# Kernel tuning notes

Measured on AMD Instinct MI355X. Metric: run time of the kernel, lower is better.

## Reference

```python
import jax, jax.numpy as jnp
import numpy as np

B, S1, S2, C = 8, 256, 256, 64
M1, M2 = 32, 32          # n_modes per spatial dim
SCALE = 1.0 / (C * C)    # 1/(in_channels*out_channels)


def setup_inputs() -> dict:
    key = jax.random.key(0)
    ks = jax.random.split(key, 5)
    X = jax.random.normal(ks[0], (B, S1, S2, C), dtype=jnp.float32)
    k0r = SCALE * jax.random.normal(ks[1], (M1, C, C), dtype=jnp.float32)
    k0i = SCALE * jax.random.normal(ks[2], (M1, C, C), dtype=jnp.float32)
    k1r = SCALE * jax.random.normal(ks[3], (M2, C, C), dtype=jnp.float32)
    k1i = SCALE * jax.random.normal(ks[4], (M2, C, C), dtype=jnp.float32)
    return {"X": X, "k0r": k0r, "k0i": k0i, "k1r": k1r, "k1i": k1i}


def reference(X, k0r, k0i, k1r, k1i):
    # Factorized spectral conv: per-spatial-dim rFFT -> truncated-mode
    # complex channel mix -> zero-pad -> irFFT, summed over dims.
    k0 = jax.lax.complex(k0r, k0i)  # (M1, out, in)
    k1 = jax.lax.complex(k1r, k1i)  # (M2, out, in)

    out = jnp.zeros_like(X)

    # --- spatial dim 0 (axis -3) ---
    Xf = jnp.fft.rfft(X, axis=-3, norm="forward")          # (B, S1//2+1, S2, C) complex
    Yt = jnp.einsum("rij,bryj->bryi", k0, Xf[:, :M1])       # truncated-mode channel mix
    Y = jnp.zeros_like(Xf).at[:, :M1].set(Yt)               # zero-pad back to full modes
    out = out + jnp.fft.irfft(Y, n=S1, axis=-3, norm="forward")

    # --- spatial dim 1 (axis -2) ---
    Xf = jnp.fft.rfft(X, axis=-2, norm="forward")           # (B, S1, S2//2+1, C)
    Yt = jnp.einsum("rij,bxrj->bxri", k1, Xf[:, :, :M2])
    Y = jnp.zeros_like(Xf).at[:, :, :M2].set(Yt)
    out = out + jnp.fft.irfft(Y, n=S2, axis=-2, norm="forward")

    return out
```

## Files before the change

### kernel.cpp

```cpp
#include <hip/hip_runtime.h>


namespace {

constexpr int S = 256, C = 64;

typedef _Float16 f16;
typedef _Float16 f16x2 __attribute__((ext_vector_type(2)));
typedef _Float16 f16x4 __attribute__((ext_vector_type(4)));
typedef _Float16 f16x8 __attribute__((ext_vector_type(8)));
typedef float f32x16 __attribute__((ext_vector_type(16)));

constexpr int OFF_FWDF = 0;
constexpr int OFF_INVF = 8192;
constexpr int OFF_A2   = 16384;

constexpr int P   = 4624;
constexpr int XFO = 8 * P;
constexpr int LDS_BYTES = 16 * P;

__device__ __host__ inline int cadr(int c) { return c * 16 + (c >> 3) * 16; }

__global__ void k_init_all(const float* __restrict__ k0r, const float* __restrict__ k0i,
                           const float* __restrict__ k1r, const float* __restrict__ ki1,
                           float* __restrict__ ws) {
  const int bid = blockIdx.x;
  if (bid < 128) {
    int t = bid * 256 + threadIdx.x;
    f16* fwdF = (f16*)(ws + OFF_FWDF);
    f16* invF = (f16*)(ws + OFF_INVF);
    if (t < 16384) {
      int e = t & 7, lane = (t >> 3) & 63, mtkk = t >> 9;
      int mt = mtkk & 1, kk = mtkk >> 1;
      int mc = mt * 32 + (lane & 31);
      int x = kk * 16 + 8 * (lane >> 5) + e;
      int r = mc >> 1;
      double ang = (double)((r * x) & 255) * (3.14159265358979323846 / 128.0);
      double v = (mc & 1) ? -sin(ang) : cos(ang);
      fwdF[t] = (f16)(float)v;
    } else {
      int t2 = t - 16384;
      int e = t2 & 7, lane = (t2 >> 3) & 63, mtg = (t2 >> 9) & 7, kk = t2 >> 12;
      int u = mtg * 32 + (lane & 31);
      int mcv = kk * 16 + 8 * (lane >> 5) + e;
      int r = mcv >> 1;
      double wgt = (r == 0) ? 1.0 : 2.0;
      double ang = (double)((r * u) & 255) * (3.14159265358979323846 / 128.0);
      double v = (mcv & 1) ? -wgt * sin(ang) : wgt * cos(ang);
      invF[t2] = (f16)(float)(v * (1.0 / 256.0));
    }
    return;
  }
  const int db = bid - 128;
  const float* kr = (db < 2048) ? k0r : k1r;
  const float* ki = (db < 2048) ? k0i : ki1;
  f16* A2 = (f16*)(ws + OFF_A2) + ((db < 2048) ? 0 : 524288);
  int t = (db & 2047) * 256 + threadIdx.x;
  int e = t & 7, l = (t >> 3) & 63, kk = (t >> 9) & 7, mt = (t >> 12) & 3, r = t >> 14;
  int m = mt * 32 + (l & 31);
  int kreal = kk * 16 + 8 * (l >> 5) + e;
  int i = m >> 1, imo = m & 1, j = kreal >> 1, imi = kreal & 1;
  int src = (r * 64 + i) * 64 + j;
  float v = (imi == 0) ? ((imo == 0) ? kr[src] : ki[src])
                       : ((imo == 0) ? -ki[src] : kr[src]);
  A2[t] = (f16)v;
}

template <int DIM>
__launch_bounds__(512, 2)
__global__ void k_dim(const float* __restrict__ X, const float* __restrict__ ws,
                      float* __restrict__ out) {
  __shared__ char sm[LDS_BYTES] __attribute__((aligned(16)));

  const int tid = threadIdx.x;
  const int l = tid & 63, w = tid >> 6;
  const int g2 = l >> 5, l31 = l & 31;
  const int n0 = w * 32;
  const int b = blockIdx.x >> 6;
  const int t4 = (blockIdx.x & 63) * 4;
  const size_t bbase = (size_t)b * (S * S * C);
  const f16* fwdF = (const f16*)(ws + OFF_FWDF);
  const f16* invF = (const f16*)(ws + OFF_INVF);
  const f16* A2 = (const f16*)(ws + OFF_A2) + (DIM == 0 ? 0 : 524288);

  auto gofs = [&](int u, int c) -> size_t {
    if (DIM == 0)
      return bbase + (size_t)u * (S * C) + (size_t)(t4 + (c >> 6)) * C + (c & 63);
    else
      return bbase + (size_t)(t4 + (c >> 6)) * (S * C) + (size_t)u * C + (c & 63);
  };

  const int ug = w >> 1;
  const int c1 = (w & 1) * 128 + l;
  const int c2 = c1 + 64;

  float r1[8], r2[8];
  auto stage_load = [&](int u0) {
#pragma unroll
    for (int j = 0; j < 8; ++j) r1[j] = X[gofs(u0 + ug * 8 + j, c1)];
#pragma unroll
    for (int j = 0; j < 8; ++j) r2[j] = X[gofs(u0 + ug * 8 + j, c2)];
  };
  auto stage_write = [&](int buf) {
    f16x8 v1, v2;
#pragma unroll
    for (int j = 0; j < 8; ++j) { v1[j] = (f16)r1[j]; v2[j] = (f16)r2[j]; }
    char* base = sm + buf * (4 * P) + ug * P;
    *(f16x8*)(base + cadr(c1)) = v1;
    *(f16x8*)(base + cadr(c2)) = v2;
  };

  f32x16 acc0, acc1;
#pragma unroll
  for (int q = 0; q < 16; ++q) { acc0[q] = 0.f; acc1[q] = 0.f; }

  stage_load(0);
  stage_write(0);
  __syncthreads();

  for (int ch = 0; ch < 8; ++ch) {
    if (ch < 7) stage_load((ch + 1) * 32);
    const char* bbuf = sm + (ch & 1) * (4 * P);
#pragma unroll
    for (int ks = 0; ks < 2; ++ks) {
      const int kk = ch * 2 + ks;
      f16x8 bf = *(const f16x8*)(bbuf + (ks * 2 + g2) * P + cadr(n0 + l31));
      f16x8 a0 = *(const f16x8*)(fwdF + ((size_t)(kk * 2 + 0) * 64 + l) * 8);
      f16x8 a1 = *(const f16x8*)(fwdF + ((size_t)(kk * 2 + 1) * 64 + l) * 8);
      acc0 = __builtin_amdgcn_mfma_f32_32x32x16_f16(a0, bf, acc0, 0, 0, 0);
      acc1 = __builtin_amdgcn_mfma_f32_32x32x16_f16(a1, bf, acc1, 0, 0, 0);
    }
    if (ch < 7) {
      stage_write((ch + 1) & 1);
      __syncthreads();
    }
  }
  __syncthreads();

  {
    const int col = n0 + l31;
    const int p = col >> 6, j = col & 63;
    const int kk = j >> 3, g2p = (j >> 2) & 1, js = j & 3;
#pragma unroll
    for (int pr = 0; pr < 16; ++pr) {
      const int q = (pr & 7) >> 1, hf = pr & 1;
      const int r = 2 * g2 + 4 * q + hf + (pr >> 3) * 16;
      const int reg = 4 * q + 2 * hf;
      const float v0 = (pr < 8) ? acc0[reg] : acc1[reg];
      const float v1 = (pr < 8) ? acc0[reg + 1] : acc1[reg + 1];
      f16x2 v2 = {(f16)v0, (f16)v1};
      const int W = (r * 16 + kk * 2 + g2p) * 4 + p;
      *(f16x2*)(sm + W * 16 + (W >> 3) * 16 + js * 4) = v2;
    }
  }
  __syncthreads();

  {
    const int colsel = l31 & 3;
#pragma unroll 1
    for (int rq = 0; rq < 4; ++rq) {
      const int r = w * 4 + rq;
      f16x8 bfr[8];
#pragma unroll
      for (int kk = 0; kk < 8; ++kk) {
        const int W = (r * 16 + kk * 2 + g2) * 4 + colsel;
        bfr[kk] = *(const f16x8*)(sm + W * 16 + (W >> 3) * 16);
      }
      char* yb = sm + XFO + w * P;
      const int ebyte = rq * 4;
#pragma unroll 1
      for (int mt = 0; mt < 4; ++mt) {
        f32x16 acc;
#pragma unroll
        for (int q = 0; q < 16; ++q) acc[q] = 0.f;
#pragma unroll
        for (int kk = 0; kk < 8; ++kk) {
          f16x8 af = *(const f16x8*)(A2 + ((size_t)((r * 4 + mt) * 8 + kk) * 64 + l) * 8);
          acc = __builtin_amdgcn_mfma_f32_32x32x16_f16(af, bfr[kk], acc, 0, 0, 0);
        }
        if (l31 < 4) {
#pragma unroll
          for (int t2 = 0; t2 < 8; ++t2) {
            int reg = t2 * 2;
            int rowin = (reg & 3) + 8 * (reg >> 2) + 4 * g2;
            int i = (mt * 32 + rowin) >> 1;
            f16x2 v2 = {(f16)acc[reg], (f16)acc[reg + 1]};
            *(f16x2*)(yb + cadr(l31 * 64 + i) + ebyte) = v2;
          }
        }
      }
    }
  }
  __syncthreads();

  const int colg = n0 + l31;
  const int pp = colg >> 6, jj = colg & 63;
  f16x8 bf4[4];
#pragma unroll
  for (int kk = 0; kk < 4; ++kk)
    bf4[kk] = *(const f16x8*)(sm + XFO + (kk * 2 + g2) * P + cadr(colg));

#pragma unroll 1
  for (int h = 0; h < 2; ++h) {
#pragma unroll 1
    for (int mt = 0; mt < 4; ++mt) {
      f32x16 a4;
#pragma unroll
      for (int q = 0; q < 16; ++q) a4[q] = 0.f;

#pragma unroll
      for (int kk = 0; kk < 4; ++kk) {
        f16x8 A = *(const f16x8*)(invF + ((size_t)(kk * 8 + h * 4 + mt) * 64 + l) * 8);
        a4 = __builtin_amdgcn_mfma_f32_32x32x16_f16(A, bf4[kk], a4, 0, 0, 0);
      }

      const int u0 = (h * 4 + mt) * 32;
#pragma unroll
      for (int reg = 0; reg < 16; ++reg) {
        const int u = u0 + (reg & 3) + 8 * (reg >> 2) + 4 * g2;
        size_t g = (DIM == 0)
                       ? bbase + (size_t)u * (S * C) + (size_t)(t4 + pp) * C + jj
                       : bbase + (size_t)(t4 + pp) * (S * C) + (size_t)u * C + jj;
        if (DIM == 0) out[g] = a4[reg];
        else          out[g] += a4[reg];
      }
    }
  }
}

}

extern "C" void kernel_launch(void* const* d_in, const int* in_sizes, int n_in,
                              void* d_out, int out_size, void* d_ws, size_t ws_size,
                              hipStream_t stream) {
  (void)in_sizes; (void)n_in; (void)out_size; (void)ws_size;
  const float* X   = (const float*)d_in[0];
  const float* k0r = (const float*)d_in[1];
  const float* k0i = (const float*)d_in[2];
  const float* k1r = (const float*)d_in[3];
  const float* k1i = (const float*)d_in[4];
  float* out = (float*)d_out;
  float* ws  = (float*)d_ws;

  k_init_all<<<4224, 256, 0, stream>>>(k0r, k0i, k1r, k1i, ws);
  k_dim<0><<<512, 512, 0, stream>>>(X, ws, out);
  k_dim<1><<<512, 512, 0, stream>>>(X, ws, out);
}
```

Measured before the change: 161.5 us.

## Stage dim-0 partial output in fp16 workspace and reverse dim-1 block order

When the workspace is large enough, the dim-0 pass writes its result as fp16 into the workspace, and the dim-1 pass reads that partial and writes the final output once. This replaces the fp32 read-modify-write of the output. The dim-1 grid is traversed in reverse order so its first blocks touch data the dim-0 pass wrote last, which may still be in cache. The twiddle-table init switches from double to float trig, and staging the partial in fp16 adds rounding error to the sum.

New measurement: 149.5 us. 7.4% less time.

```diff
diff --git a/kernel.cpp b/kernel.cpp
--- a/kernel.cpp
+++ b/kernel.cpp
@@ -14,6 +14,8 @@
 constexpr int OFF_FWDF = 0;
 constexpr int OFF_INVF = 8192;
 constexpr int OFF_A2   = 16384;
+constexpr int OFF_PW   = 540672;
+constexpr size_t WS_NEED = (size_t)OFF_PW * 4 + (size_t)8 * 256 * 256 * 64 * 2;
 
 constexpr int P   = 4624;
 constexpr int XFO = 8 * P;
@@ -35,19 +37,19 @@
       int mc = mt * 32 + (lane & 31);
       int x = kk * 16 + 8 * (lane >> 5) + e;
       int r = mc >> 1;
-      double ang = (double)((r * x) & 255) * (3.14159265358979323846 / 128.0);
-      double v = (mc & 1) ? -sin(ang) : cos(ang);
-      fwdF[t] = (f16)(float)v;
+      float ang = (float)((r * x) & 255) * (3.14159265358979323846f / 128.0f);
+      float v = (mc & 1) ? -sinf(ang) : cosf(ang);
+      fwdF[t] = (f16)v;
     } else {
       int t2 = t - 16384;
       int e = t2 & 7, lane = (t2 >> 3) & 63, mtg = (t2 >> 9) & 7, kk = t2 >> 12;
       int u = mtg * 32 + (lane & 31);
       int mcv = kk * 16 + 8 * (lane >> 5) + e;
       int r = mcv >> 1;
-      double wgt = (r == 0) ? 1.0 : 2.0;
-      double ang = (double)((r * u) & 255) * (3.14159265358979323846 / 128.0);
-      double v = (mcv & 1) ? -wgt * sin(ang) : wgt * cos(ang);
-      invF[t2] = (f16)(float)(v * (1.0 / 256.0));
+      float wgt = (r == 0) ? 1.0f : 2.0f;
+      float ang = (float)((r * u) & 255) * (3.14159265358979323846f / 128.0f);
+      float v = (mcv & 1) ? -wgt * sinf(ang) : wgt * cosf(ang);
+      invF[t2] = (f16)(v * (1.0f / 256.0f));
     }
     return;
   }
@@ -66,18 +68,20 @@
   A2[t] = (f16)v;
 }
 
-template <int DIM>
+template <int MODE>
 __launch_bounds__(512, 2)
 __global__ void k_dim(const float* __restrict__ X, const float* __restrict__ ws,
-                      float* __restrict__ out) {
+                      float* __restrict__ out, f16* __restrict__ pw) {
+  constexpr int DIM = (MODE == 0 || MODE == 2) ? 0 : 1;
   __shared__ char sm[LDS_BYTES] __attribute__((aligned(16)));
 
   const int tid = threadIdx.x;
   const int l = tid & 63, w = tid >> 6;
   const int g2 = l >> 5, l31 = l & 31;
   const int n0 = w * 32;
-  const int b = blockIdx.x >> 6;
-  const int t4 = (blockIdx.x & 63) * 4;
+  const int bid = (DIM == 1) ? (int)(gridDim.x - 1 - blockIdx.x) : (int)blockIdx.x;
+  const int b = bid >> 6;
+  const int t4 = (bid & 63) * 4;
   const size_t bbase = (size_t)b * (S * S * C);
   const f16* fwdF = (const f16*)(ws + OFF_FWDF);
   const f16* invF = (const f16*)(ws + OFF_INVF);
@@ -221,8 +225,10 @@
         size_t g = (DIM == 0)
                        ? bbase + (size_t)u * (S * C) + (size_t)(t4 + pp) * C + jj
                        : bbase + (size_t)(t4 + pp) * (S * C) + (size_t)u * C + jj;
-        if (DIM == 0) out[g] = a4[reg];
-        else          out[g] += a4[reg];
+        if (MODE == 0) out[g] = a4[reg];
+        else if (MODE == 1) out[g] += a4[reg];
+        else if (MODE == 2) pw[g] = (f16)a4[reg];
+        else out[g] = a4[reg] + (float)pw[g];
       }
     }
   }
@@ -233,7 +239,7 @@
 extern "C" void kernel_launch(void* const* d_in, const int* in_sizes, int n_in,
                               void* d_out, int out_size, void* d_ws, size_t ws_size,
                               hipStream_t stream) {
-  (void)in_sizes; (void)n_in; (void)out_size; (void)ws_size;
+  (void)in_sizes; (void)n_in; (void)out_size;
   const float* X   = (const float*)d_in[0];
   const float* k0r = (const float*)d_in[1];
   const float* k0i = (const float*)d_in[2];
@@ -241,8 +247,14 @@
   const float* k1i = (const float*)d_in[4];
   float* out = (float*)d_out;
   float* ws  = (float*)d_ws;
+  f16* pw = (f16*)(ws + OFF_PW);
 
   k_init_all<<<4224, 256, 0, stream>>>(k0r, k0i, k1r, k1i, ws);
-  k_dim<0><<<512, 512, 0, stream>>>(X, ws, out);
-  k_dim<1><<<512, 512, 0, stream>>>(X, ws, out);
-}
+  if (ws_size >= WS_NEED) {
+    k_dim<2><<<512, 512, 0, stream>>>(X, ws, out, pw);
+    k_dim<3><<<512, 512, 0, stream>>>(X, ws, out, pw);
+  } else {
+    k_dim<0><<<512, 512, 0, stream>>>(X, ws, out, nullptr);
+    k_dim<1><<<512, 512, 0, stream>>>(X, ws, out, nullptr);
+  }
+}
```
